# Performance work log

Hardware: AMD Instinct MI355X
Metric: run time of the kernel (lower is better)

The kernel has to match this reference:

```python
import jax, jax.numpy as jnp
import numpy as np

N, E = 50000, 640000
IN, HD, OUT, NCLS = 768, 128, 128, 2
H, C = 4, 32  # heads, per-head channels (HD/H = OUT/H = 32)
NEG_SLOPE = 0.2


def _glorot(key, shape):
    fan_in, fan_out = shape[0], shape[1]
    lim = jnp.sqrt(6.0 / (fan_in + fan_out))
    return jax.random.uniform(key, shape, jnp.float32, -lim, lim)


def setup_inputs() -> dict:
    key = jax.random.key(0)
    ks = jax.random.split(key, 24)
    x = jax.random.normal(ks[0], (1, N, IN), jnp.float32)
    edge_index = jax.random.randint(ks[1], (2, E), 0, N, jnp.int64)
    d = {"x": x, "edge_index": edge_index}
    ins = [IN, HD, HD, HD]
    for i in range(4):
        d[f"Wl{i+1}"] = _glorot(ks[2 + 5 * i], (ins[i], H * C))
        d[f"Wr{i+1}"] = _glorot(ks[3 + 5 * i], (ins[i], H * C))
        d[f"att{i+1}"] = _glorot(ks[4 + 5 * i], (H, C))
        d[f"b{i+1}"] = jnp.zeros((H * C,), jnp.float32)
    d["clfW"] = _glorot(ks[22], (OUT, NCLS))
    d["clfb"] = jnp.zeros((NCLS,), jnp.float32)
    return d


def _gatv2_layer(x, Wl, Wr, att, b, src, dst):
    # x: [N, F_in] -> out: [N, H*C]. GATv2: e = a^T LeakyReLU(xl_j + xr_i)
    xl = (x @ Wl).reshape(N, H, C)
    xr = (x @ Wr).reshape(N, H, C)
    h = xl[src] + xr[dst]                                   # [E', H, C] per-edge gather
    e = jnp.einsum('ehc,hc->eh', jax.nn.leaky_relu(h, NEG_SLOPE), att)
    m = jax.ops.segment_max(e, dst, num_segments=N)          # scatter-softmax (stable)
    a = jnp.exp(e - m[dst])
    s = jax.ops.segment_sum(a, dst, num_segments=N)
    alpha = a / (s[dst] + 1e-16)
    out = jax.ops.segment_sum(alpha[..., None] * xl[src], dst, num_segments=N)
    return out.reshape(N, H * C) + b


def reference(x, edge_index, Wl1, Wr1, att1, b1, Wl2, Wr2, att2, b2,
              Wl3, Wr3, att3, b3, Wl4, Wr4, att4, b4, clfW, clfb):
    xn = x.reshape(N, IN)  # torch.squeeze
    loops = jnp.arange(N, dtype=edge_index.dtype)  # PyG add_self_loops=True
    src = jnp.concatenate([edge_index[0], loops])
    dst = jnp.concatenate([edge_index[1], loops])
    h = jax.nn.relu(_gatv2_layer(xn, Wl1, Wr1, att1, b1, src, dst))
    h = jax.nn.relu(_gatv2_layer(h, Wl2, Wr2, att2, b2, src, dst))
    h = jax.nn.relu(_gatv2_layer(h, Wl3, Wr3, att3, b3, src, dst))
    h = _gatv2_layer(h, Wl4, Wr4, att4, b4, src, dst)        # [N, OUT]
    g = jnp.mean(h, axis=0, keepdims=True)                   # unsqueeze+mean over nodes -> [1, OUT]
    return g @ clfW + clfb                                   # [1, NCLS]
```

## Files before the change

kernel.cpp:

```cpp
#include <hip/hip_runtime.h>
#include <hip/hip_bf16.h>

#define NN 50000
#define EE 640000
#define HC 128
#define NB1 196

typedef short bf16x8 __attribute__((ext_vector_type(8)));
typedef float f32x4 __attribute__((ext_vector_type(4)));
typedef unsigned short u16;

__device__ __forceinline__ u16 f2b(float f) {
    unsigned u = __float_as_uint(f);
    unsigned r = u + 0x7FFFu + ((u >> 16) & 1u);
    return (u16)(r >> 16);
}
__device__ __forceinline__ float b2f(u16 h) {
    return __uint_as_float(((unsigned)h) << 16);
}

__device__ __forceinline__ void gload_lds16(const void* g, void* l) {
    __builtin_amdgcn_global_load_lds((const __attribute__((address_space(1))) void*)g,
                                     (__attribute__((address_space(3))) void*)l, 16, 0, 0);
}

__device__ __forceinline__ float red16(float x) {
    x += __int_as_float(__builtin_amdgcn_update_dpp(0, __float_as_int(x), 0xB1, 0xF, 0xF, true));
    x += __int_as_float(__builtin_amdgcn_update_dpp(0, __float_as_int(x), 0x4E, 0xF, 0xF, true));
    x += __int_as_float(__builtin_amdgcn_update_dpp(0, __float_as_int(x), 0x141, 0xF, 0xF, true));
    x += __int_as_float(__builtin_amdgcn_update_dpp(0, __float_as_int(x), 0x128, 0xF, 0xF, true));
    return x;
}


__global__ void k_count(const int* __restrict__ ei, int* __restrict__ cnt) {
    int e = blockIdx.x * blockDim.x + threadIdx.x;
    if (e < EE) atomicAdd(&cnt[ei[EE + e]], 1);
}

__global__ void k_bsum(const int* __restrict__ cnt, int* __restrict__ bsum) {
    __shared__ int sd[256];
    int b = blockIdx.x, t = threadIdx.x, i = b * 256 + t;
    sd[t] = (i < NN) ? cnt[i] + 1 : 0;
    __syncthreads();
    for (int o = 128; o; o >>= 1) { if (t < o) sd[t] += sd[t + o]; __syncthreads(); }
    if (!t) bsum[b] = sd[0];
}

__global__ void k_bscan(const int* __restrict__ bsum, int* __restrict__ bex,
                        int* __restrict__ offs) {
    __shared__ int sd[256];
    int t = threadIdx.x;
    int v = (t < NB1) ? bsum[t] : 0;
    sd[t] = v; __syncthreads();
    for (int o = 1; o < 256; o <<= 1) {
        int u = (t >= o) ? sd[t - o] : 0;
        __syncthreads(); sd[t] += u; __syncthreads();
    }
    bex[t] = sd[t] - v;
    if (t == NB1 - 1) offs[NN] = sd[t];
}

__global__ void k_offs(const int* __restrict__ cnt_in, const int* __restrict__ bex,
                       int* __restrict__ offs, int* __restrict__ cursor,
                       int* __restrict__ csr) {
    __shared__ int sd[256];
    int b = blockIdx.x, t = threadIdx.x, i = b * 256 + t;
    int v = (i < NN) ? cnt_in[i] + 1 : 0;
    sd[t] = v; __syncthreads();
    for (int o = 1; o < 256; o <<= 1) {
        int u = (t >= o) ? sd[t - o] : 0;
        __syncthreads(); sd[t] += u; __syncthreads();
    }
    if (i < NN) {
        int o = bex[b] + sd[t] - v;
        offs[i] = o;
        csr[o] = i;
        cursor[i] = o + 1;
    }
}

__global__ void k_fill(const int* __restrict__ ei, int* __restrict__ cursor,
                       int* __restrict__ csr) {
    int e = blockIdx.x * blockDim.x + threadIdx.x;
    if (e < EE) {
        int s = ei[e], d = ei[EE + e];
        int pos = atomicAdd(&cursor[d], 1);
        csr[pos] = s;
    }
}


#define WT_L0 196608
#define WT_LX 32768
#define WT_TOT (WT_L0 + 3 * WT_LX)

__global__ void k_castw_all(const float* __restrict__ Wl1, const float* __restrict__ Wr1,
                            const float* __restrict__ Wl2, const float* __restrict__ Wr2,
                            const float* __restrict__ Wl3, const float* __restrict__ Wr3,
                            const float* __restrict__ Wl4, const float* __restrict__ Wr4,
                            u16* __restrict__ WtAll) {
    int gid = blockIdx.x * 256 + threadIdx.x;
    if (gid >= WT_TOT) return;
    const float *Wl, *Wr;
    int idx, K, base;
    if (gid < WT_L0) { Wl = Wl1; Wr = Wr1; idx = gid; K = 768; base = 0; }
    else {
        int r = gid - WT_L0;
        int l = r >> 15; idx = r & (WT_LX - 1); K = 128; base = WT_L0 + l * WT_LX;
        if (l == 0)      { Wl = Wl2; Wr = Wr2; }
        else if (l == 1) { Wl = Wl3; Wr = Wr3; }
        else             { Wl = Wl4; Wr = Wr4; }
    }
    int c = idx / K, k = idx - c * K;
    float v = (c < 128) ? Wl[k * 128 + c] : Wr[k * 128 + (c - 128)];
    WtAll[base + idx] = f2b(v);
}


template<int K, bool F32A>
__global__ __launch_bounds__(256)
void k_gemm(const void* __restrict__ Ag, const u16* __restrict__ Wt,
            u16* __restrict__ xb) {
    __shared__ __align__(16) u16 As[64 * 64];
    __shared__ __align__(16) u16 Bs[256 * 64];
    const int tid = threadIdx.x;
    const int wv = tid >> 6, ln = tid & 63;
    const int m0 = blockIdx.x * 64;
    const int lrow = ln & 15, g = ln >> 4;

    f32x4 acc[4][4] = {};

    const float* Af = (const float*)Ag;
    const u16* Ab = (const u16*)Ag;
    const int arow = tid >> 2, aq = tid & 3;
    int arg = m0 + arow; if (arg >= NN) arg = 0;
    float4 ra0, ra1, ra2, ra3;

    if constexpr (F32A) {
        const float* src = Af + (size_t)arg * K + aq * 16;
        ra0 = *(const float4*)(src);
        ra1 = *(const float4*)(src + 4);
        ra2 = *(const float4*)(src + 8);
        ra3 = *(const float4*)(src + 12);
    }

    constexpr int NSTEP = K / 64;
    for (int ks = 0; ks < NSTEP; ++ks) {
        if constexpr (F32A) {
            const int s = arow & 7;
            bf16x8 v0, v1;
            v0[0] = (short)f2b(ra0.x); v0[1] = (short)f2b(ra0.y);
            v0[2] = (short)f2b(ra0.z); v0[3] = (short)f2b(ra0.w);
            v0[4] = (short)f2b(ra1.x); v0[5] = (short)f2b(ra1.y);
            v0[6] = (short)f2b(ra1.z); v0[7] = (short)f2b(ra1.w);
            v1[0] = (short)f2b(ra2.x); v1[1] = (short)f2b(ra2.y);
            v1[2] = (short)f2b(ra2.z); v1[3] = (short)f2b(ra2.w);
            v1[4] = (short)f2b(ra3.x); v1[5] = (short)f2b(ra3.y);
            v1[6] = (short)f2b(ra3.z); v1[7] = (short)f2b(ra3.w);
            *(bf16x8*)&As[arow * 64 + (((aq * 2) ^ s) * 8)] = v0;
            *(bf16x8*)&As[arow * 64 + (((aq * 2 + 1) ^ s) * 8)] = v1;
        } else {
            #pragma unroll
            for (int q = 0; q < 2; ++q) {
                int r8 = (wv * 2 + q) * 8;
                int row = r8 + (ln >> 3);
                int lc = (ln & 7) ^ (row & 7);
                int rg = m0 + row; if (rg >= NN) rg = 0;
                gload_lds16(Ab + (size_t)rg * K + ks * 64 + lc * 8, &As[r8 * 64]);
            }
        }
        #pragma unroll
        for (int q = 0; q < 8; ++q) {
            int r8 = (wv * 8 + q) * 8;
            int row = r8 + (ln >> 3);
            int lc = (ln & 7) ^ (row & 7);
            gload_lds16(Wt + (size_t)row * K + ks * 64 + lc * 8, &Bs[r8 * 64]);
        }
        __syncthreads();

        if constexpr (F32A) {
            if (ks + 1 < NSTEP) {
                const float* src = Af + (size_t)arg * K + (ks + 1) * 64 + aq * 16;
                ra0 = *(const float4*)(src);
                ra1 = *(const float4*)(src + 4);
                ra2 = *(const float4*)(src + 8);
                ra3 = *(const float4*)(src + 12);
            }
        }

        #pragma unroll
        for (int kk = 0; kk < 2; ++kk) {
            bf16x8 af[4], bfr[4];
            #pragma unroll
            for (int f = 0; f < 4; ++f) {
                int r = f * 16 + lrow;
                af[f] = *(const bf16x8*)&As[r * 64 + (((kk * 4 + g) ^ (r & 7)) * 8)];
                int c = wv * 64 + f * 16 + lrow;
                bfr[f] = *(const bf16x8*)&Bs[c * 64 + (((kk * 4 + g) ^ (c & 7)) * 8)];
            }
            #pragma unroll
            for (int i = 0; i < 4; ++i)
                #pragma unroll
                for (int j = 0; j < 4; ++j)
                    acc[i][j] = __builtin_amdgcn_mfma_f32_16x16x32_bf16(af[i], bfr[j], acc[i][j], 0, 0, 0);
        }
        __syncthreads();
    }

    const int crow0 = m0 + (g << 2);
    const int ccol0 = wv * 64 + lrow;
    #pragma unroll
    for (int i = 0; i < 4; ++i)
        #pragma unroll
        for (int rr = 0; rr < 4; ++rr) {
            int row = crow0 + i * 16 + rr;
            if (row < NN) {
                #pragma unroll
                for (int j = 0; j < 4; ++j)
                    xb[(size_t)row * 256 + ccol0 + j * 16] = f2b(acc[i][j][rr]);
            }
        }
}


__global__ __launch_bounds__(256)
void k_edge(const u16* __restrict__ xb, const float* __restrict__ att,
            const float* __restrict__ bias, const int* __restrict__ offs,
            const int* __restrict__ csr, u16* __restrict__ outb,
            float* __restrict__ outf, int relu) {
    int i = blockIdx.x * 4 + (threadIdx.x >> 6);
    if (i >= NN) return;
    int ln = threadIdx.x & 63;
    int ch0 = ((ln >> 4) << 5) + ((ln & 15) << 1);

    unsigned xr2 = *(const unsigned*)&xb[(size_t)i * 256 + 128 + ch0];
    float xri0 = b2f((u16)xr2), xri1 = b2f((u16)(xr2 >> 16));
    float2 atv = *(const float2*)&att[ch0];
    const float at0 = atv.x, at1 = atv.y;
    int beg = offs[i];
    int deg = offs[i + 1] - beg;

    float m0v = -3.0e38f, s0v = 0.f, p00 = 0.f, p01 = 0.f;
    float m1v = -3.0e38f, s1v = 0.f, p10 = 0.f, p11 = 0.f;
    float m2v = -3.0e38f, s2v = 0.f, p20 = 0.f, p21 = 0.f;
    float m3v = -3.0e38f, s3v = 0.f, p30 = 0.f, p31 = 0.f;

#define GATH(k, jj) unsigned w##k = *(const unsigned*)&xb[(size_t)(jj) * 256 + ch0];
#define UPD(k, M, S, A0, A1) { \
    float v0 = b2f((u16)w##k), v1 = b2f((u16)(w##k >> 16)); \
    float u0 = v0 + xri0; u0 = (u0 > 0.f) ? u0 : 0.2f * u0; \
    float u1 = v1 + xri1; u1 = (u1 > 0.f) ? u1 : 0.2f * u1; \
    float e = red16(u0 * at0 + u1 * at1); \
    float mn = fmaxf(M, e); float c = __expf(M - mn), ww = __expf(e - mn); \
    S = S * c + ww; A0 = A0 * c + ww * v0; A1 = A1 * c + ww * v1; M = mn; }

    for (int base = 0; base < deg; base += 64) {
        int lim = deg - base; if (lim > 64) lim = 64;
        int idxv = (base + ln < deg) ? csr[beg + base + ln] : 0;
        int p = 0;
        for (; p + 4 <= lim; p += 4) {
            int j0 = __shfl(idxv, p);
            int j1 = __shfl(idxv, p + 1);
            int j2 = __shfl(idxv, p + 2);
            int j3 = __shfl(idxv, p + 3);
            GATH(0, j0) GATH(1, j1) GATH(2, j2) GATH(3, j3)
            UPD(0, m0v, s0v, p00, p01)
            UPD(1, m1v, s1v, p10, p11)
            UPD(2, m2v, s2v, p20, p21)
            UPD(3, m3v, s3v, p30, p31)
        }
        for (; p < lim; ++p) {
            int j0 = __shfl(idxv, p);
            GATH(4, j0)
            UPD(4, m0v, s0v, p00, p01)
        }
    }
#undef GATH
#undef UPD

    float mm = fmaxf(fmaxf(m0v, m1v), fmaxf(m2v, m3v));
    float c0 = __expf(m0v - mm), c1 = __expf(m1v - mm);
    float c2 = __expf(m2v - mm), c3 = __expf(m3v - mm);
    float s = s0v * c0 + s1v * c1 + s2v * c2 + s3v * c3 + 1e-16f;
    float inv = 1.f / s;
    float2 bv = *(const float2*)&bias[ch0];
    float o0 = (p00 * c0 + p10 * c1 + p20 * c2 + p30 * c3) * inv + bv.x;
    float o1 = (p01 * c0 + p11 * c1 + p21 * c2 + p31 * c3) * inv + bv.y;
    if (relu) { o0 = fmaxf(o0, 0.f); o1 = fmaxf(o1, 0.f); }
    if (outb) {
        unsigned pk = (unsigned)f2b(o0) | ((unsigned)f2b(o1) << 16);
        *(unsigned*)&outb[(size_t)i * HC + ch0] = pk;
    }
    if (outf) {
        *(float2*)&outf[(size_t)i * HC + ch0] = make_float2(o0, o1);
    }
}


__global__ __launch_bounds__(256)
void k_colsum(const float* __restrict__ h, float* __restrict__ gsum) {
    __shared__ float4 sd[8][32];
    int t = threadIdx.x;
    int c4 = t & 31, rl = t >> 5;
    float sx = 0.f, sy = 0.f, sz = 0.f, sw = 0.f;
    for (int r = blockIdx.x * 8 + rl; r < NN; r += 8 * gridDim.x) {
        float4 v = *(const float4*)&h[(size_t)r * HC + c4 * 4];
        sx += v.x; sy += v.y; sz += v.z; sw += v.w;
    }
    sd[rl][c4] = make_float4(sx, sy, sz, sw);
    __syncthreads();
    if (rl == 0) {
        float4 a = sd[0][c4];
        #pragma unroll
        for (int q = 1; q < 8; ++q) {
            float4 b = sd[q][c4];
            a.x += b.x; a.y += b.y; a.z += b.z; a.w += b.w;
        }
        atomicAdd(&gsum[c4 * 4 + 0], a.x);
        atomicAdd(&gsum[c4 * 4 + 1], a.y);
        atomicAdd(&gsum[c4 * 4 + 2], a.z);
        atomicAdd(&gsum[c4 * 4 + 3], a.w);
    }
}

__global__ void k_clf(const float* __restrict__ gsum, const float* __restrict__ W,
                      const float* __restrict__ bcls, float* __restrict__ out) {
    __shared__ float v[HC];
    int t = threadIdx.x;
    v[t] = gsum[t] * (1.f / (float)NN);
    __syncthreads();
    if (t < 2) {
        float r = 0.f;
        for (int k = 0; k < HC; ++k) r += v[k] * W[k * 2 + t];
        out[t] = r + bcls[t];
    }
}


extern "C" void kernel_launch(void* const* d_in, const int* in_sizes, int n_in,
                              void* d_out, int out_size, void* d_ws, size_t ws_size,
                              hipStream_t stream) {
    const float* x = (const float*)d_in[0];
    const int* ei = (const int*)d_in[1];
    const float *Wl[4], *Wr[4], *att[4], *bia[4];
    for (int l = 0; l < 4; ++l) {
        Wl[l] = (const float*)d_in[2 + 4 * l];
        Wr[l] = (const float*)d_in[3 + 4 * l];
        att[l] = (const float*)d_in[4 + 4 * l];
        bia[l] = (const float*)d_in[5 + 4 * l];
    }
    const float* clfW = (const float*)d_in[18];
    const float* clfb = (const float*)d_in[19];
    float* outp = (float*)d_out;

    char* w = (char*)d_ws;
    size_t o = 0;
    auto alloc = [&](size_t bytes) {
        char* p = w + o;
        o = (o + bytes + 255) & ~(size_t)255;
        return p;
    };
    int* cnt    = (int*)alloc((size_t)NN * 4);
    float* gsum = (float*)alloc(HC * 4);
    size_t zspan = o;
    int* offs  = (int*)alloc((size_t)(NN + 1) * 4);
    int* csr   = (int*)alloc((size_t)(EE + NN) * 4);
    int* bsum  = (int*)alloc((size_t)NB1 * 4);
    int* bex   = (int*)alloc(256 * 4);
    u16* WtAll = (u16*)alloc((size_t)WT_TOT * 2);
    u16* xb    = (u16*)alloc((size_t)NN * 256 * 2);
    u16* hb0   = (u16*)alloc((size_t)NN * HC * 2);
    u16* hb1   = (u16*)alloc((size_t)NN * HC * 2);
    float* hfin = (float*)alloc((size_t)NN * HC * 4);

    hipMemsetAsync(cnt, 0, zspan, stream);
    k_count<<<(EE + 255) / 256, 256, 0, stream>>>(ei, cnt);
    k_bsum<<<NB1, 256, 0, stream>>>(cnt, bsum);
    k_bscan<<<1, 256, 0, stream>>>(bsum, bex, offs);
    k_offs<<<NB1, 256, 0, stream>>>(cnt, bex, offs, cnt, csr);
    k_fill<<<(EE + 255) / 256, 256, 0, stream>>>(ei, cnt, csr);
    k_castw_all<<<(WT_TOT + 255) / 256, 256, 0, stream>>>(
        Wl[0], Wr[0], Wl[1], Wr[1], Wl[2], Wr[2], Wl[3], Wr[3], WtAll);

    const int GB = (NN + 63) / 64;
    const u16* Wt_l[4] = {WtAll, WtAll + WT_L0, WtAll + WT_L0 + WT_LX,
                          WtAll + WT_L0 + 2 * WT_LX};
    const u16* hb_in = nullptr;
    u16* hbb[2] = {hb0, hb1};
    for (int l = 0; l < 4; ++l) {
        if (l == 0) k_gemm<768, true ><<<GB, 256, 0, stream>>>((const void*)x, Wt_l[0], xb);
        else        k_gemm<128, false><<<GB, 256, 0, stream>>>((const void*)hb_in, Wt_l[l], xb);
        u16* ob = (l < 3) ? hbb[l & 1] : nullptr;
        float* of = (l == 3) ? hfin : nullptr;
        k_edge<<<(NN + 3) / 4, 256, 0, stream>>>(xb, att[l], bia[l], offs, csr, ob, of,
                                                 (l < 3) ? 1 : 0);
        hb_in = ob;
    }

    k_colsum<<<504, 256, 0, stream>>>(hfin, gsum);
    k_clf<<<1, 128, 0, stream>>>(gsum, clfW, clfb, outp);
}
```

Before: 417.4 us.

## Double-buffer GEMM K-loop, fuse block scan into offsets, cheaper online softmax

The GEMM now uses K-steps of 32 with double-buffered LDS tiles, issuing the next tile's loads before the current MFMAs, and requests four blocks per CU through launch bounds. The separate single-block scan kernel is removed: each offsets block scans the block sums itself, saving one launch. The edge kernel's online-softmax update computes one exp instead of two, and LeakyReLU becomes an fmax. Costs are redundant scan work in every block, smaller K-steps with more barriers, and register pressure from the occupancy hint.

```diff
diff --git a/kernel.cpp b/kernel.cpp
--- a/kernel.cpp
+++ b/kernel.cpp
@@ -47,37 +47,31 @@
     if (!t) bsum[b] = sd[0];
 }
 
-__global__ void k_bscan(const int* __restrict__ bsum, int* __restrict__ bex,
-                        int* __restrict__ offs) {
-    __shared__ int sd[256];
-    int t = threadIdx.x;
-    int v = (t < NB1) ? bsum[t] : 0;
-    sd[t] = v; __syncthreads();
-    for (int o = 1; o < 256; o <<= 1) {
-        int u = (t >= o) ? sd[t - o] : 0;
-        __syncthreads(); sd[t] += u; __syncthreads();
-    }
-    bex[t] = sd[t] - v;
-    if (t == NB1 - 1) offs[NN] = sd[t];
-}
-
-__global__ void k_offs(const int* __restrict__ cnt_in, const int* __restrict__ bex,
+__global__ void k_offs(const int* __restrict__ cnt_in, const int* __restrict__ bsum,
                        int* __restrict__ offs, int* __restrict__ cursor,
                        int* __restrict__ csr) {
+    __shared__ int sb[256];
     __shared__ int sd[256];
     int b = blockIdx.x, t = threadIdx.x, i = b * 256 + t;
+    sb[t] = (t < NB1) ? bsum[t] : 0;
     int v = (i < NN) ? cnt_in[i] + 1 : 0;
-    sd[t] = v; __syncthreads();
+    sd[t] = v;
+    __syncthreads();
     for (int o = 1; o < 256; o <<= 1) {
-        int u = (t >= o) ? sd[t - o] : 0;
-        __syncthreads(); sd[t] += u; __syncthreads();
-    }
+        int u1 = (t >= o) ? sd[t - o] : 0;
+        int u2 = (t >= o) ? sb[t - o] : 0;
+        __syncthreads();
+        sd[t] += u1; sb[t] += u2;
+        __syncthreads();
+    }
+    int bex = (b > 0) ? sb[b - 1] : 0;
     if (i < NN) {
-        int o = bex[b] + sd[t] - v;
+        int o = bex + sd[t] - v;
         offs[i] = o;
         csr[o] = i;
         cursor[i] = o + 1;
     }
+    if (b == NB1 - 1 && t == 0) offs[NN] = sb[NB1 - 1];
 }
 
 __global__ void k_fill(const int* __restrict__ ei, int* __restrict__ cursor,
@@ -119,15 +113,16 @@
 
 
 template<int K, bool F32A>
-__global__ __launch_bounds__(256)
+__global__ __launch_bounds__(256, 4)
 void k_gemm(const void* __restrict__ Ag, const u16* __restrict__ Wt,
             u16* __restrict__ xb) {
-    __shared__ __align__(16) u16 As[64 * 64];
-    __shared__ __align__(16) u16 Bs[256 * 64];
+    __shared__ __align__(16) u16 As[2][64 * 32];
+    __shared__ __align__(16) u16 Bs[2][256 * 32];
     const int tid = threadIdx.x;
     const int wv = tid >> 6, ln = tid & 63;
     const int m0 = blockIdx.x * 64;
     const int lrow = ln & 15, g = ln >> 4;
+    constexpr int NSTEP = K / 32;
 
     f32x4 acc[4][4] = {};
 
@@ -135,78 +130,68 @@
     const u16* Ab = (const u16*)Ag;
     const int arow = tid >> 2, aq = tid & 3;
     int arg = m0 + arow; if (arg >= NN) arg = 0;
-    float4 ra0, ra1, ra2, ra3;
+    const int alc = aq ^ ((arow >> 1) & 3);
+    float4 rx, ry;
+
+#define LOADREGS(ks) { const float* s_ = Af + (size_t)arg * K + (ks) * 32 + aq * 8; \
+                       rx = *(const float4*)(s_); ry = *(const float4*)(s_ + 4); }
+#define WRITEA(c) { bf16x8 v_; \
+        v_[0] = (short)f2b(rx.x); v_[1] = (short)f2b(rx.y); \
+        v_[2] = (short)f2b(rx.z); v_[3] = (short)f2b(rx.w); \
+        v_[4] = (short)f2b(ry.x); v_[5] = (short)f2b(ry.y); \
+        v_[6] = (short)f2b(ry.z); v_[7] = (short)f2b(ry.w); \
+        *(bf16x8*)&As[c][arow * 32 + alc * 8] = v_; }
+#define STAGEB(ks, c) { \
+        _Pragma("unroll") \
+        for (int q = 0; q < 4; ++q) { \
+            int seg = (wv * 4 + q) * 64 + ln; \
+            int row = seg >> 2, cc = seg & 3; \
+            int lc = cc ^ ((row >> 1) & 3); \
+            gload_lds16(Wt + (size_t)row * K + (ks) * 32 + lc * 8, &Bs[c][(wv * 4 + q) * 512]); \
+        } }
+#define STAGEAB(ks, c) gload_lds16(Ab + (size_t)arg * K + (ks) * 32 + alc * 8, &As[c][wv * 512]);
 
     if constexpr (F32A) {
-        const float* src = Af + (size_t)arg * K + aq * 16;
-        ra0 = *(const float4*)(src);
-        ra1 = *(const float4*)(src + 4);
-        ra2 = *(const float4*)(src + 8);
-        ra3 = *(const float4*)(src + 12);
-    }
-
-    constexpr int NSTEP = K / 64;
-    for (int ks = 0; ks < NSTEP; ++ks) {
-        if constexpr (F32A) {
-            const int s = arow & 7;
-            bf16x8 v0, v1;
-            v0[0] = (short)f2b(ra0.x); v0[1] = (short)f2b(ra0.y);
-            v0[2] = (short)f2b(ra0.z); v0[3] = (short)f2b(ra0.w);
-            v0[4] = (short)f2b(ra1.x); v0[5] = (short)f2b(ra1.y);
-            v0[6] = (short)f2b(ra1.z); v0[7] = (short)f2b(ra1.w);
-            v1[0] = (short)f2b(ra2.x); v1[1] = (short)f2b(ra2.y);
-            v1[2] = (short)f2b(ra2.z); v1[3] = (short)f2b(ra2.w);
-            v1[4] = (short)f2b(ra3.x); v1[5] = (short)f2b(ra3.y);
-            v1[6] = (short)f2b(ra3.z); v1[7] = (short)f2b(ra3.w);
-            *(bf16x8*)&As[arow * 64 + (((aq * 2) ^ s) * 8)] = v0;
-            *(bf16x8*)&As[arow * 64 + (((aq * 2 + 1) ^ s) * 8)] = v1;
-        } else {
+        LOADREGS(0)
+        WRITEA(0)
+        STAGEB(0, 0)
+        if (NSTEP > 1) LOADREGS(1)
+    } else {
+        STAGEAB(0, 0)
+        STAGEB(0, 0)
+    }
+    __syncthreads();
+
+    for (int t = 0; t < NSTEP; ++t) {
+        const int c = t & 1;
+        if (t + 1 < NSTEP) {
+            STAGEB(t + 1, c ^ 1)
+            if constexpr (F32A) {
+                WRITEA(c ^ 1)
+                if (t + 2 < NSTEP) LOADREGS(t + 2)
+            } else {
+                STAGEAB(t + 1, c ^ 1)
+            }
+        }
+        bf16x8 af[4], bfr[4];
+        #pragma unroll
+        for (int f = 0; f < 4; ++f) {
+            int r = f * 16 + lrow;
+            af[f] = *(const bf16x8*)&As[c][r * 32 + ((g ^ ((r >> 1) & 3)) * 8)];
+            int cr = wv * 64 + f * 16 + lrow;
+            bfr[f] = *(const bf16x8*)&Bs[c][cr * 32 + ((g ^ ((cr >> 1) & 3)) * 8)];
+        }
+        #pragma unroll
+        for (int i = 0; i < 4; ++i)
             #pragma unroll
-            for (int q = 0; q < 2; ++q) {
-                int r8 = (wv * 2 + q) * 8;
-                int row = r8 + (ln >> 3);
-                int lc = (ln & 7) ^ (row & 7);
-                int rg = m0 + row; if (rg >= NN) rg = 0;
-                gload_lds16(Ab + (size_t)rg * K + ks * 64 + lc * 8, &As[r8 * 64]);
-            }
-        }
-        #pragma unroll
-        for (int q = 0; q < 8; ++q) {
-            int r8 = (wv * 8 + q) * 8;
-            int row = r8 + (ln >> 3);
-            int lc = (ln & 7) ^ (row & 7);
-            gload_lds16(Wt + (size_t)row * K + ks * 64 + lc * 8, &Bs[r8 * 64]);
-        }
-        __syncthreads();
-
-        if constexpr (F32A) {
-            if (ks + 1 < NSTEP) {
-                const float* src = Af + (size_t)arg * K + (ks + 1) * 64 + aq * 16;
-                ra0 = *(const float4*)(src);
-                ra1 = *(const float4*)(src + 4);
-                ra2 = *(const float4*)(src + 8);
-                ra3 = *(const float4*)(src + 12);
-            }
-        }
-
-        #pragma unroll
-        for (int kk = 0; kk < 2; ++kk) {
-            bf16x8 af[4], bfr[4];
-            #pragma unroll
-            for (int f = 0; f < 4; ++f) {
-                int r = f * 16 + lrow;
-                af[f] = *(const bf16x8*)&As[r * 64 + (((kk * 4 + g) ^ (r & 7)) * 8)];
-                int c = wv * 64 + f * 16 + lrow;
-                bfr[f] = *(const bf16x8*)&Bs[c * 64 + (((kk * 4 + g) ^ (c & 7)) * 8)];
-            }
-            #pragma unroll
-            for (int i = 0; i < 4; ++i)
-                #pragma unroll
-                for (int j = 0; j < 4; ++j)
-                    acc[i][j] = __builtin_amdgcn_mfma_f32_16x16x32_bf16(af[i], bfr[j], acc[i][j], 0, 0, 0);
-        }
-        __syncthreads();
-    }
+            for (int j = 0; j < 4; ++j)
+                acc[i][j] = __builtin_amdgcn_mfma_f32_16x16x32_bf16(af[i], bfr[j], acc[i][j], 0, 0, 0);
+        if (t + 1 < NSTEP) __syncthreads();
+    }
+#undef LOADREGS
+#undef WRITEA
+#undef STAGEB
+#undef STAGEAB
 
     const int crow0 = m0 + (g << 2);
     const int ccol0 = wv * 64 + lrow;
@@ -249,11 +234,16 @@
 #define GATH(k, jj) unsigned w##k = *(const unsigned*)&xb[(size_t)(jj) * 256 + ch0];
 #define UPD(k, M, S, A0, A1) { \
     float v0 = b2f((u16)w##k), v1 = b2f((u16)(w##k >> 16)); \
-    float u0 = v0 + xri0; u0 = (u0 > 0.f) ? u0 : 0.2f * u0; \
-    float u1 = v1 + xri1; u1 = (u1 > 0.f) ? u1 : 0.2f * u1; \
+    float u0 = v0 + xri0; u0 = fmaxf(u0, 0.2f * u0); \
+    float u1 = v1 + xri1; u1 = fmaxf(u1, 0.2f * u1); \
     float e = red16(u0 * at0 + u1 * at1); \
-    float mn = fmaxf(M, e); float c = __expf(M - mn), ww = __expf(e - mn); \
-    S = S * c + ww; A0 = A0 * c + ww * v0; A1 = A1 * c + ww * v1; M = mn; }
+    float d = e - M; \
+    float tt = __expf(-fabsf(d)); \
+    bool ng = (d <= 0.f); \
+    float c = ng ? 1.f : tt; \
+    float ww = ng ? tt : 1.f; \
+    M = ng ? M : e; \
+    S = S * c + ww; A0 = A0 * c + ww * v0; A1 = A1 * c + ww * v1; }
 
     for (int base = 0; base < deg; base += 64) {
         int lim = deg - base; if (lim > 64) lim = 64;
@@ -367,7 +357,6 @@
     int* offs  = (int*)alloc((size_t)(NN + 1) * 4);
     int* csr   = (int*)alloc((size_t)(EE + NN) * 4);
     int* bsum  = (int*)alloc((size_t)NB1 * 4);
-    int* bex   = (int*)alloc(256 * 4);
     u16* WtAll = (u16*)alloc((size_t)WT_TOT * 2);
     u16* xb    = (u16*)alloc((size_t)NN * 256 * 2);
     u16* hb0   = (u16*)alloc((size_t)NN * HC * 2);
@@ -377,8 +366,7 @@
     hipMemsetAsync(cnt, 0, zspan, stream);
     k_count<<<(EE + 255) / 256, 256, 0, stream>>>(ei, cnt);
     k_bsum<<<NB1, 256, 0, stream>>>(cnt, bsum);
-    k_bscan<<<1, 256, 0, stream>>>(bsum, bex, offs);
-    k_offs<<<NB1, 256, 0, stream>>>(cnt, bex, offs, cnt, csr);
+    k_offs<<<NB1, 256, 0, stream>>>(cnt, bsum, offs, cnt, csr);
     k_fill<<<(EE + 255) / 256, 256, 0, stream>>>(ei, cnt, csr);
     k_castw_all<<<(WT_TOT + 255) / 256, 256, 0, stream>>>(
         Wl[0], Wr[0], Wl[1], Wr[1], Wl[2], Wr[2], Wl[3], Wr[3], WtAll);
```

New measurement: 388.8 us. 1.07x faster.
